# Performance work log

Hardware: AMD Instinct MI355X
Metric: run time of the kernel (lower is better)

The kernel has to match this reference:

```python
import jax, jax.numpy as jnp
import numpy as np

B, T, IN_DIM, OUT_DIM, H = 4096, 256, 64, 32, 128

def _linear_params(key, out_f, in_f):
    k1, k2 = jax.random.split(key)
    bound = 1.0 / np.sqrt(in_f)
    W = jax.random.uniform(k1, (out_f, in_f), jnp.float32, -bound, bound)
    b = jax.random.uniform(k2, (out_f,), jnp.float32, -bound, bound)
    return W, b

def _lstm_params(key, input_sz, hidden_sz):
    ks = jax.random.split(key, 4)
    bound = 1.0 / np.sqrt(hidden_sz)
    Wih = jax.random.uniform(ks[0], (4 * hidden_sz, input_sz), jnp.float32, -bound, bound)
    Whh = jax.random.uniform(ks[1], (4 * hidden_sz, hidden_sz), jnp.float32, -bound, bound)
    bih = jax.random.uniform(ks[2], (4 * hidden_sz,), jnp.float32, -bound, bound)
    bhh = jax.random.uniform(ks[3], (4 * hidden_sz,), jnp.float32, -bound, bound)
    return Wih, Whh, bih, bhh

def setup_inputs() -> dict:
    key = jax.random.key(0)
    ks = jax.random.split(key, 9)
    seq = jax.random.normal(ks[0], (B, T, IN_DIM), jnp.float32)
    h1 = jnp.zeros((B, H), jnp.float32); c1 = jnp.zeros((B, H), jnp.float32)
    h2 = jnp.zeros((B, H), jnp.float32); c2 = jnp.zeros((B, H), jnp.float32)
    W_in1, b_in1 = _linear_params(ks[1], 256, IN_DIM)
    W_in2, b_in2 = _linear_params(ks[2], 128, 256)
    W_in3, b_in3 = _linear_params(ks[3], 128, 128)
    Wih1, Whh1, bih1, bhh1 = _lstm_params(ks[4], 128, H)
    Wih2, Whh2, bih2, bhh2 = _lstm_params(ks[5], 128, H)
    W_out1, b_out1 = _linear_params(ks[6], 128, 128)
    W_out2, b_out2 = _linear_params(ks[7], 256, 128)
    W_out3, b_out3 = _linear_params(ks[8], OUT_DIM, 256)
    return dict(seq=seq, h1=h1, c1=c1, h2=h2, c2=c2,
                W_in1=W_in1, b_in1=b_in1, W_in2=W_in2, b_in2=b_in2, W_in3=W_in3, b_in3=b_in3,
                Wih1=Wih1, Whh1=Whh1, bih1=bih1, bhh1=bhh1,
                Wih2=Wih2, Whh2=Whh2, bih2=bih2, bhh2=bhh2,
                W_out1=W_out1, b_out1=b_out1, W_out2=W_out2, b_out2=b_out2, W_out3=W_out3, b_out3=b_out3)

def _lstm_cell(x, h, c, Wih, Whh, bih, bhh):
    # PyTorch LSTMCell: gates ordered i, f, g, o
    g = x @ Wih.T + bih + h @ Whh.T + bhh
    i, f, gg, o = jnp.split(g, 4, axis=-1)
    c_new = jax.nn.sigmoid(f) * c + jax.nn.sigmoid(i) * jnp.tanh(gg)
    h_new = jax.nn.sigmoid(o) * jnp.tanh(c_new)
    return h_new, c_new

def reference(seq, h1, c1, h2, c2,
              W_in1, b_in1, W_in2, b_in2, W_in3, b_in3,
              Wih1, Whh1, bih1, bhh1, Wih2, Whh2, bih2, bhh2,
              W_out1, b_out1, W_out2, b_out2, W_out3, b_out3):
    # fc_in applied to all timesteps at once (same math as per-step)
    x = jax.nn.relu(seq @ W_in1.T + b_in1)
    x = jax.nn.relu(x @ W_in2.T + b_in2)
    x = jax.nn.relu(x @ W_in3.T + b_in3)  # [B, T, 128]

    def step(carry, xt):
        h1, c1, h2, c2 = carry
        h1, c1 = _lstm_cell(xt, h1, c1, Wih1, Whh1, bih1, bhh1)
        h2, c2 = _lstm_cell(h1, h2, c2, Wih2, Whh2, bih2, bhh2)
        return (h1, c1, h2, c2), None

    (h1, c1, h2, c2), _ = jax.lax.scan(step, (h1, c1, h2, c2), jnp.swapaxes(x, 0, 1))

    y = jax.nn.relu(h2 @ W_out1.T + b_out1)
    y = jax.nn.relu(y @ W_out2.T + b_out2)
    return y @ W_out3.T + b_out3  # [B, out_dim]
```

## Files before the change

kernel.cpp:

```cpp
#include <hip/hip_runtime.h>


typedef unsigned short u16;
typedef short bf16x8 __attribute__((ext_vector_type(8)));
typedef float f32x4 __attribute__((ext_vector_type(4)));
typedef unsigned short u16x4 __attribute__((ext_vector_type(4)));

#define MFMA16(a, b, c) __builtin_amdgcn_mfma_f32_16x16x32_bf16((a), (b), (c), 0, 0, 0)

#define GLOAD_LDS(gp, lp) __builtin_amdgcn_global_load_lds( \
    (const __attribute__((address_space(1))) unsigned int*)(const void*)(gp), \
    (__attribute__((address_space(3))) unsigned int*)(void*)(lp), 16, 0, 0)

#define LGKM_BAR do { \
  asm volatile("s_waitcnt lgkmcnt(0)" ::: "memory"); \
  __builtin_amdgcn_sched_barrier(0); \
  __builtin_amdgcn_s_barrier(); \
  __builtin_amdgcn_sched_barrier(0); \
} while (0)

__device__ __forceinline__ u16 f2bf(float f) {
  union { float f; unsigned u; } v; v.f = f;
  return (u16)((v.u + 0x7FFFu + ((v.u >> 16) & 1u)) >> 16);
}
__device__ __forceinline__ float b2f(u16 v) {
  union { unsigned u; float f; } x; x.u = ((unsigned)v) << 16; return x.f;
}
__device__ __forceinline__ float fsig(float x) { return 1.0f / (1.0f + __expf(-x)); }
__device__ __forceinline__ float ftanh(float x) { return 2.0f / (1.0f + __expf(-2.0f * x)) - 1.0f; }

#define WHH1_U  0
#define WIH2_U  65536
#define WHH2_U  131072
#define WIH1_U  196608
#define W1_U    262144
#define W2_U    278528
#define W3_U    311296
#define WO1_U   327680
#define WO2_U   344064
#define WO3_U   376832
#define BS1_F   192512
#define BS2_F   193024
#define STH1_U  393216
#define STH2_U  917504
#define C1_F    720896
#define C2_F    1245184
#define G1X_U   4194304
#define TC      32
#define NCH     8


__global__ void prep_kernel(const float* __restrict__ Wih1, const float* __restrict__ Whh1,
                            const float* __restrict__ bih1, const float* __restrict__ bhh1,
                            const float* __restrict__ Wih2, const float* __restrict__ Whh2,
                            const float* __restrict__ bih2, const float* __restrict__ bhh2,
                            const float* __restrict__ W_in1, const float* __restrict__ W_in2,
                            const float* __restrict__ W_in3,
                            const float* __restrict__ W_out1, const float* __restrict__ W_out2,
                            const float* __restrict__ W_out3,
                            const float* __restrict__ h1_in, const float* __restrict__ h2_in,
                            const float* __restrict__ c1_in, const float* __restrict__ c2_in,
                            u16* __restrict__ wsu) {
  float* wsf = (float*)wsu;
  const int N_total = 2490368;
  int stride = gridDim.x * blockDim.x;
  for (int idx = blockIdx.x * blockDim.x + threadIdx.x; idx < N_total; idx += stride) {
    if (idx < 385024) {
      int within = idx & 511;
      int f = idx >> 9;
      int lane = within >> 3, e = within & 7;
      int lr = lane & 15, lg = lane >> 4;
      int k8 = lg * 8 + e;
      float v;
      if (f < 128) {
        int kf = f & 3, g = (f >> 2) & 3, w = f >> 4;
        v = Whh1[(g * 128 + w * 16 + lr) * 128 + kf * 32 + k8];
      } else if (f < 256) {
        int ff = f - 128; int kf = ff & 3, g = (ff >> 2) & 3, w = ff >> 4;
        v = Wih2[(g * 128 + w * 16 + lr) * 128 + kf * 32 + k8];
      } else if (f < 384) {
        int ff = f - 256; int kf = ff & 3, g = (ff >> 2) & 3, w = ff >> 4;
        v = Whh2[(g * 128 + w * 16 + lr) * 128 + kf * 32 + k8];
      } else if (f < 512) {
        int ff = f - 384; int kf = ff & 3, n = ff >> 2;
        v = Wih1[(n * 16 + lr) * 128 + kf * 32 + k8];
      } else if (f < 544) {
        int ff = f - 512; int kf = ff & 1, n = ff >> 1;
        v = W_in1[(n * 16 + lr) * 64 + kf * 32 + k8];
      } else if (f < 608) {
        int ff = f - 544; int kf = ff & 7, n = ff >> 3;
        v = W_in2[(n * 16 + lr) * 256 + kf * 32 + k8];
      } else if (f < 640) {
        int ff = f - 608; int kf = ff & 3, n = ff >> 2;
        v = W_in3[(n * 16 + lr) * 128 + kf * 32 + k8];
      } else if (f < 672) {
        int ff = f - 640; int kf = ff & 3, n = ff >> 2;
        v = W_out1[(n * 16 + lr) * 128 + kf * 32 + k8];
      } else if (f < 736) {
        int ff = f - 672; int kf = ff & 3, n = ff >> 2;
        v = W_out2[(n * 16 + lr) * 128 + kf * 32 + k8];
      } else {
        int ff = f - 736; int kf = ff & 7, n = ff >> 3;
        v = W_out3[(n * 16 + lr) * 256 + kf * 32 + k8];
      }
      wsu[idx] = f2bf(v);
    } else if (idx < 385536) {
      int i = idx - 385024; wsf[BS1_F + i] = bih1[i] + bhh1[i];
    } else if (idx < 386048) {
      int i = idx - 385536; wsf[BS2_F + i] = bih2[i] + bhh2[i];
    } else if (idx < 393216) {
    } else if (idx < 917504) {
      int i = idx - 393216; wsu[STH1_U + i] = f2bf(h1_in[i]);
    } else if (idx < 1441792) {
      int i = idx - 917504; wsu[STH2_U + i] = f2bf(h2_in[i]);
    } else if (idx < 1966080) {
      int i = idx - 1441792; wsf[C1_F + i] = c1_in[i];
    } else {
      int i = idx - 1966080; wsf[C2_F + i] = c2_in[i];
    }
  }
}

__global__ __launch_bounds__(256, 2)
void fc_chunk(const float* __restrict__ seq,
              const float* __restrict__ b_in1, const float* __restrict__ b_in2,
              const float* __restrict__ b_in3,
              u16* __restrict__ wsu, int t0) {
  __shared__ u16 SEQs[4096];
  __shared__ u16 F1s[16384];
  __shared__ u16 F2s[8192];
  __shared__ u16 XLs[8192];
  const int tid = threadIdx.x;
  const int wid = tid >> 6, lane = tid & 63;
  const int lr = lane & 15, lg = lane >> 4;
  const int bid_t = blockIdx.x & 1, bid_b = blockIdx.x >> 1;
  const int b0c = bid_b * 4, t0c = t0 + bid_t * 16;
  const float* bs1f = (const float*)wsu + BS1_F;

#pragma unroll
  for (int i = 0; i < 4; ++i) {
    int f = i * 1024 + tid * 4;
    int rho = f >> 6, k = f & 63;
    int b = b0c + (rho >> 4), tt = t0c + (rho & 15);
    float4 v = *(const float4*)(seq + ((size_t)b * 256 + tt) * 64 + k);
    u16x4 o = { f2bf(v.x), f2bf(v.y), f2bf(v.z), f2bf(v.w) };
    *(u16x4*)&SEQs[(rho * 64 + k) ^ ((rho & 7) << 3)] = o;
  }
  __syncthreads();

  {
    f32x4 a1[4][4] = {};
#pragma unroll
    for (int kf = 0; kf < 2; ++kf) {
      bf16x8 A[4];
#pragma unroll
      for (int rt = 0; rt < 4; ++rt) {
        int r = 16 * rt + lr;
        A[rt] = *(const bf16x8*)&SEQs[(r * 64 + (kf * 4 + lg) * 8) ^ ((r & 7) << 3)];
      }
#pragma unroll
      for (int n = 0; n < 4; ++n) {
        bf16x8 B = *(const bf16x8*)(wsu + W1_U + (size_t)(((4 * wid + n) * 2 + kf) * 512) + lane * 8);
#pragma unroll
        for (int rt = 0; rt < 4; ++rt) a1[rt][n] = MFMA16(A[rt], B, a1[rt][n]);
      }
    }
#pragma unroll
    for (int n = 0; n < 4; ++n) {
      float bb = b_in1[(4 * wid + n) * 16 + lr];
#pragma unroll
      for (int rt = 0; rt < 4; ++rt)
#pragma unroll
        for (int j = 0; j < 4; ++j) {
          int r = 16 * rt + lg * 4 + j, c = (4 * wid + n) * 16 + lr;
          F1s[(r * 256 + c) ^ ((r & 7) << 3)] = f2bf(fmaxf(a1[rt][n][j] + bb, 0.f));
        }
    }
  }
  __syncthreads();

  {
    f32x4 a2[4][2] = {};
#pragma unroll
    for (int kf = 0; kf < 8; ++kf) {
      bf16x8 A[4];
#pragma unroll
      for (int rt = 0; rt < 4; ++rt) {
        int r = 16 * rt + lr;
        A[rt] = *(const bf16x8*)&F1s[(r * 256 + (kf * 4 + lg) * 8) ^ ((r & 7) << 3)];
      }
#pragma unroll
      for (int n = 0; n < 2; ++n) {
        bf16x8 B = *(const bf16x8*)(wsu + W2_U + (size_t)(((2 * wid + n) * 8 + kf) * 512) + lane * 8);
#pragma unroll
        for (int rt = 0; rt < 4; ++rt) a2[rt][n] = MFMA16(A[rt], B, a2[rt][n]);
      }
    }
#pragma unroll
    for (int n = 0; n < 2; ++n) {
      float bb = b_in2[(2 * wid + n) * 16 + lr];
#pragma unroll
      for (int rt = 0; rt < 4; ++rt)
#pragma unroll
        for (int j = 0; j < 4; ++j) {
          int r = 16 * rt + lg * 4 + j, c = (2 * wid + n) * 16 + lr;
          F2s[(r * 128 + c) ^ ((r & 7) << 3)] = f2bf(fmaxf(a2[rt][n][j] + bb, 0.f));
        }
    }
  }
  __syncthreads();

  {
    f32x4 a3[4][2] = {};
#pragma unroll
    for (int kf = 0; kf < 4; ++kf) {
      bf16x8 A[4];
#pragma unroll
      for (int rt = 0; rt < 4; ++rt) {
        int r = 16 * rt + lr;
        A[rt] = *(const bf16x8*)&F2s[(r * 128 + (kf * 4 + lg) * 8) ^ ((r & 7) << 3)];
      }
#pragma unroll
      for (int n = 0; n < 2; ++n) {
        bf16x8 B = *(const bf16x8*)(wsu + W3_U + (size_t)(((2 * wid + n) * 4 + kf) * 512) + lane * 8);
#pragma unroll
        for (int rt = 0; rt < 4; ++rt) a3[rt][n] = MFMA16(A[rt], B, a3[rt][n]);
      }
    }
#pragma unroll
    for (int n = 0; n < 2; ++n) {
      float bb = b_in3[(2 * wid + n) * 16 + lr];
#pragma unroll
      for (int rt = 0; rt < 4; ++rt)
#pragma unroll
        for (int j = 0; j < 4; ++j) {
          int r = 16 * rt + lg * 4 + j, c = (2 * wid + n) * 16 + lr;
          XLs[(r * 128 + c) ^ ((r & 7) << 3)] = f2bf(fmaxf(a3[rt][n][j] + bb, 0.f));
        }
    }
  }
  __syncthreads();

  {
    f32x4 a4[4][8] = {};
#pragma unroll
    for (int kf = 0; kf < 4; ++kf) {
      bf16x8 A[4];
#pragma unroll
      for (int rt = 0; rt < 4; ++rt) {
        int r = 16 * rt + lr;
        A[rt] = *(const bf16x8*)&XLs[(r * 128 + (kf * 4 + lg) * 8) ^ ((r & 7) << 3)];
      }
#pragma unroll
      for (int n = 0; n < 8; ++n) {
        bf16x8 B = *(const bf16x8*)(wsu + WIH1_U + (size_t)(((wid * 8 + n) * 4 + kf) * 512) + lane * 8);
#pragma unroll
        for (int rt = 0; rt < 4; ++rt) a4[rt][n] = MFMA16(A[rt], B, a4[rt][n]);
      }
    }
    const int blk = bid_b >> 2, slg = bid_b & 3;
#pragma unroll
    for (int n = 0; n < 8; ++n) {
      float bb = bs1f[(wid * 8 + n) * 16 + lr];
#pragma unroll
      for (int j = 0; j < 4; ++j) {
        int tl = bid_t * 16 + lg * 4 + j;
        u16x4 o = { f2bf(a4[0][n][j] + bb), f2bf(a4[1][n][j] + bb),
                    f2bf(a4[2][n][j] + bb), f2bf(a4[3][n][j] + bb) };
        size_t au = (size_t)G1X_U +
            ((((((size_t)tl * 256 + blk) * 4 + slg) * 4 + wid) * 8 + n) * 16 + lr) * 4;
        *(u16x4*)(wsu + au) = o;
      }
    }
  }
}

__global__ __launch_bounds__(512, 1)
void scan_chunk(u16* __restrict__ wsu, float* __restrict__ out,
                const float* __restrict__ b_out1, const float* __restrict__ b_out2,
                const float* __restrict__ b_out3, int last) {
  __shared__ u16 Wl[65536];
  __shared__ u16 H1d[2][2048], H2d[2][2048];

  float* wsf = (float*)wsu;
  const int tid = threadIdx.x;
  const int wid = tid >> 6, lane = tid & 63;
  const int lr = lane & 15, lg = lane >> 4;
  const int b0 = blockIdx.x * 16;
  const int blkid = blockIdx.x;
  const int r5 = tid >> 5, c5 = (tid & 31) * 4;
  const int swl = (r5 * 128 + c5) ^ ((r5 & 7) << 3);

  bf16x8 wA[4][4], wB[4][4];
#pragma unroll
  for (int g = 0; g < 4; ++g)
#pragma unroll
    for (int kf = 0; kf < 4; ++kf) {
      wA[g][kf] = *(const bf16x8*)(wsu + WHH1_U + (size_t)(((wid * 4 + g) * 4 + kf) * 512) + lane * 8);
      wB[g][kf] = *(const bf16x8*)(wsu + WIH2_U + (size_t)(((wid * 4 + g) * 4 + kf) * 512) + lane * 8);
    }
#pragma unroll
  for (int g = 0; g < 4; ++g)
#pragma unroll
    for (int kf = 0; kf < 4; ++kf) {
      asm volatile("" : "+a"(wA[g][kf]));
      asm volatile("" : "+a"(wB[g][kf]));
    }

#pragma unroll
  for (int i = 0; i < 16; ++i)
    GLOAD_LDS(wsu + WHH2_U + wid * 8192 + i * 512 + lane * 8, &Wl[wid * 8192 + i * 512]);

  *(u16x4*)&H1d[0][swl] = *(const u16x4*)(wsu + STH1_U + (size_t)(b0 + r5) * 128 + c5);
  *(u16x4*)&H2d[0][swl] = *(const u16x4*)(wsu + STH2_U + (size_t)(b0 + r5) * 128 + c5);
  float cs1[4], cs2[4], bc2[4];
#pragma unroll
  for (int j = 0; j < 4; ++j) {
    cs1[j] = wsf[C1_F + (size_t)(b0 + lg * 4 + j) * 128 + 16 * wid + lr];
    cs2[j] = wsf[C2_F + (size_t)(b0 + lg * 4 + j) * 128 + 16 * wid + lr];
  }
#pragma unroll
  for (int g = 0; g < 4; ++g) bc2[g] = wsf[BS2_F + g * 128 + 16 * wid + lr];

  u16x4 gx[4];
#pragma unroll
  for (int g = 0; g < 4; ++g)
    gx[g] = *(const u16x4*)(wsu + G1X_U +
        ((((((size_t)0 * 256 + blkid) * 4 + lg) * 4 + g) * 8 + wid) * 16 + lr) * 4);

  __syncthreads();

  auto frag = [&](const u16* buf, int kg) -> bf16x8 {
    return *(const bf16x8*)&buf[(lr * 128 + kg * 8) ^ ((lr & 7) << 3)];
  };

#pragma unroll 2
  for (int tl = 0; tl < TC; ++tl) {
    const int p = tl & 1, q = p ^ 1;

    f32x4 acc[4];
#pragma unroll
    for (int g = 0; g < 4; ++g)
      acc[g] = (f32x4){ b2f(gx[g][0]), b2f(gx[g][1]), b2f(gx[g][2]), b2f(gx[g][3]) };
    if (tl < TC - 1) {
#pragma unroll
      for (int g = 0; g < 4; ++g)
        gx[g] = *(const u16x4*)(wsu + G1X_U +
            ((((((size_t)(tl + 1) * 256 + blkid) * 4 + lg) * 4 + g) * 8 + wid) * 16 + lr) * 4);
    }
    bf16x8 h1f[4];
#pragma unroll
    for (int kf = 0; kf < 4; ++kf) h1f[kf] = frag(H1d[p], kf * 4 + lg);
#pragma unroll
    for (int kf = 0; kf < 4; ++kf)
#pragma unroll
      for (int g = 0; g < 4; ++g) acc[g] = MFMA16(h1f[kf], wA[g][kf], acc[g]);
    u16 hv[4];
#pragma unroll
    for (int j = 0; j < 4; ++j) {
      float cn = fsig(acc[1][j]) * cs1[j] + fsig(acc[0][j]) * ftanh(acc[2][j]);
      cs1[j] = cn;
      hv[j] = f2bf(fsig(acc[3][j]) * ftanh(cn));
    }
#pragma unroll
    for (int j = 0; j < 4; ++j) {
      int r = lg * 4 + j;
      H1d[q][(r * 128 + 16 * wid + lr) ^ ((r & 7) << 3)] = hv[j];
    }
    LGKM_BAR;

    f32x4 acd[4];
#pragma unroll
    for (int g = 0; g < 4; ++g) acd[g] = (f32x4){ bc2[g], bc2[g], bc2[g], bc2[g] };
#pragma unroll
    for (int kf = 0; kf < 4; ++kf) {
      bf16x8 h1n = frag(H1d[q], kf * 4 + lg);
#pragma unroll
      for (int g = 0; g < 4; ++g) acd[g] = MFMA16(h1n, wB[g][kf], acd[g]);
    }
#pragma unroll
    for (int kf = 0; kf < 4; ++kf) {
      bf16x8 h2f = frag(H2d[p], kf * 4 + lg);
#pragma unroll
      for (int g = 0; g < 4; ++g) {
        bf16x8 B = *(const bf16x8*)&Wl[((wid * 16 + g * 4 + kf) * 512) + lane * 8];
        acd[g] = MFMA16(h2f, B, acd[g]);
      }
    }
#pragma unroll
    for (int j = 0; j < 4; ++j) {
      float cn = fsig(acd[1][j]) * cs2[j] + fsig(acd[0][j]) * ftanh(acd[2][j]);
      cs2[j] = cn;
      hv[j] = f2bf(fsig(acd[3][j]) * ftanh(cn));
    }
#pragma unroll
    for (int j = 0; j < 4; ++j) {
      int r = lg * 4 + j;
      H2d[q][(r * 128 + 16 * wid + lr) ^ ((r & 7) << 3)] = hv[j];
    }
  }
  LGKM_BAR;

  if (!last) {
    *(u16x4*)(wsu + STH1_U + (size_t)(b0 + r5) * 128 + c5) = *(const u16x4*)&H1d[0][swl];
    *(u16x4*)(wsu + STH2_U + (size_t)(b0 + r5) * 128 + c5) = *(const u16x4*)&H2d[0][swl];
#pragma unroll
    for (int j = 0; j < 4; ++j) {
      wsf[C1_F + (size_t)(b0 + lg * 4 + j) * 128 + 16 * wid + lr] = cs1[j];
      wsf[C2_F + (size_t)(b0 + lg * 4 + j) * 128 + 16 * wid + lr] = cs2[j];
    }
  } else {
    {
      f32x4 y1 = {};
#pragma unroll
      for (int kf = 0; kf < 4; ++kf) {
        bf16x8 A = frag(H2d[0], kf * 4 + lg);
        bf16x8 B = *(const bf16x8*)(wsu + WO1_U + (size_t)((wid * 4 + kf) * 512) + lane * 8);
        y1 = MFMA16(A, B, y1);
      }
      float bo1 = b_out1[wid * 16 + lr];
      LGKM_BAR;
#pragma unroll
      for (int j = 0; j < 4; ++j) {
        int r = lg * 4 + j;
        H1d[1][(r * 128 + 16 * wid + lr) ^ ((r & 7) << 3)] = f2bf(fmaxf(y1[j] + bo1, 0.f));
      }
      LGKM_BAR;
    }
    {
      f32x4 y2[2] = {};
#pragma unroll
      for (int kf = 0; kf < 4; ++kf) {
        bf16x8 A = frag(H1d[1], kf * 4 + lg);
#pragma unroll
        for (int n = 0; n < 2; ++n) {
          bf16x8 B = *(const bf16x8*)(wsu + WO2_U + (size_t)(((2 * wid + n) * 4 + kf) * 512) + lane * 8);
          y2[n] = MFMA16(A, B, y2[n]);
        }
      }
      LGKM_BAR;
#pragma unroll
      for (int n = 0; n < 2; ++n)
#pragma unroll
        for (int j = 0; j < 4; ++j) {
          int c = (2 * wid + n) * 16 + lr;
          float v = fmaxf(y2[n][j] + b_out2[c], 0.f);
          u16* buf = (c < 128) ? &H2d[1][0] : &H1d[0][0];
          int cc = c & 127, r = lg * 4 + j;
          buf[(r * 128 + cc) ^ ((r & 7) << 3)] = f2bf(v);
        }
      LGKM_BAR;
    }
    if (wid < 2) {
      f32x4 y3 = {};
#pragma unroll
      for (int kf = 0; kf < 8; ++kf) {
        const u16* ab = (kf < 4) ? &H2d[1][0] : &H1d[0][0];
        bf16x8 A = frag(ab, (kf & 3) * 4 + lg);
        bf16x8 B = *(const bf16x8*)(wsu + WO3_U + (size_t)((wid * 8 + kf) * 512) + lane * 8);
        y3 = MFMA16(A, B, y3);
      }
      float bo3 = b_out3[wid * 16 + lr];
#pragma unroll
      for (int j = 0; j < 4; ++j)
        out[(size_t)(b0 + lg * 4 + j) * 32 + wid * 16 + lr] = y3[j] + bo3;
    }
  }
}

extern "C" void kernel_launch(void* const* d_in, const int* in_sizes, int n_in,
                              void* d_out, int out_size, void* d_ws, size_t ws_size,
                              hipStream_t stream) {
  (void)in_sizes; (void)n_in; (void)out_size; (void)ws_size;
  const float* seq    = (const float*)d_in[0];
  const float* h1     = (const float*)d_in[1];
  const float* c1     = (const float*)d_in[2];
  const float* h2     = (const float*)d_in[3];
  const float* c2     = (const float*)d_in[4];
  const float* W_in1  = (const float*)d_in[5];
  const float* b_in1  = (const float*)d_in[6];
  const float* W_in2  = (const float*)d_in[7];
  const float* b_in2  = (const float*)d_in[8];
  const float* W_in3  = (const float*)d_in[9];
  const float* b_in3  = (const float*)d_in[10];
  const float* Wih1   = (const float*)d_in[11];
  const float* Whh1   = (const float*)d_in[12];
  const float* bih1   = (const float*)d_in[13];
  const float* bhh1   = (const float*)d_in[14];
  const float* Wih2   = (const float*)d_in[15];
  const float* Whh2   = (const float*)d_in[16];
  const float* bih2   = (const float*)d_in[17];
  const float* bhh2   = (const float*)d_in[18];
  const float* W_out1 = (const float*)d_in[19];
  const float* b_out1 = (const float*)d_in[20];
  const float* W_out2 = (const float*)d_in[21];
  const float* b_out2 = (const float*)d_in[22];
  const float* W_out3 = (const float*)d_in[23];
  const float* b_out3 = (const float*)d_in[24];
  u16* wsu = (u16*)d_ws;
  float* out = (float*)d_out;

  hipLaunchKernelGGL(prep_kernel, dim3(512), dim3(256), 0, stream,
                     Wih1, Whh1, bih1, bhh1, Wih2, Whh2, bih2, bhh2,
                     W_in1, W_in2, W_in3, W_out1, W_out2, W_out3,
                     h1, h2, c1, c2, wsu);
  for (int k = 0; k < NCH; ++k) {
    hipLaunchKernelGGL(fc_chunk, dim3(2048), dim3(256), 0, stream,
                       seq, b_in1, b_in2, b_in3, wsu, k * TC);
    hipLaunchKernelGGL(scan_chunk, dim3(256), dim3(512), 0, stream,
                       wsu, out, b_out1, b_out2, b_out3, (k == NCH - 1) ? 1 : 0);
  }
}
```

Before: 1.924 ms.

## Move LSTM1 input projection into scan kernel and reduce chunk count

The x@Wih1 projection moves out of the FC kernel and into the recurrent scan kernel. Wih1 fragments stay resident in registers and the bf16 FC output (128 wide) is streamed into LDS with prefetch two steps ahead. The per-step gate preload from a precomputed buffer is replaced by extra MFMAs. The launch uses one or two chunks depending on workspace size instead of eight, which removes launch and state save/restore overhead, but adds 16 MFMAs per step to the serial recurrence and more register pressure.

```diff
diff --git a/kernel.cpp b/kernel.cpp
--- a/kernel.cpp
+++ b/kernel.cpp
@@ -23,16 +23,13 @@
   union { float f; unsigned u; } v; v.f = f;
   return (u16)((v.u + 0x7FFFu + ((v.u >> 16) & 1u)) >> 16);
 }
-__device__ __forceinline__ float b2f(u16 v) {
-  union { unsigned u; float f; } x; x.u = ((unsigned)v) << 16; return x.f;
-}
 __device__ __forceinline__ float fsig(float x) { return 1.0f / (1.0f + __expf(-x)); }
 __device__ __forceinline__ float ftanh(float x) { return 2.0f / (1.0f + __expf(-2.0f * x)) - 1.0f; }
 
 #define WHH1_U  0
 #define WIH2_U  65536
-#define WHH2_U  131072
-#define WIH1_U  196608
+#define WIH1_U  131072
+#define WHH2_U  196608
 #define W1_U    262144
 #define W2_U    278528
 #define W3_U    311296
@@ -45,10 +42,7 @@
 #define STH2_U  917504
 #define C1_F    720896
 #define C2_F    1245184
-#define G1X_U   4194304
-#define TC      32
-#define NCH     8
-
+#define XBUF_U  4194304
 
 __global__ void prep_kernel(const float* __restrict__ Wih1, const float* __restrict__ Whh1,
                             const float* __restrict__ bih1, const float* __restrict__ bhh1,
@@ -72,18 +66,12 @@
       int lr = lane & 15, lg = lane >> 4;
       int k8 = lg * 8 + e;
       float v;
-      if (f < 128) {
-        int kf = f & 3, g = (f >> 2) & 3, w = f >> 4;
-        v = Whh1[(g * 128 + w * 16 + lr) * 128 + kf * 32 + k8];
-      } else if (f < 256) {
-        int ff = f - 128; int kf = ff & 3, g = (ff >> 2) & 3, w = ff >> 4;
-        v = Wih2[(g * 128 + w * 16 + lr) * 128 + kf * 32 + k8];
-      } else if (f < 384) {
-        int ff = f - 256; int kf = ff & 3, g = (ff >> 2) & 3, w = ff >> 4;
-        v = Whh2[(g * 128 + w * 16 + lr) * 128 + kf * 32 + k8];
-      } else if (f < 512) {
-        int ff = f - 384; int kf = ff & 3, n = ff >> 2;
-        v = Wih1[(n * 16 + lr) * 128 + kf * 32 + k8];
+      if (f < 512) {
+        int kf = f & 3, g = (f >> 2) & 3, w = (f >> 4) & 7;
+        int row = g * 128 + w * 16 + lr;
+        int k = kf * 32 + k8;
+        const float* M = (f < 128) ? Whh1 : (f < 256) ? Wih2 : (f < 384) ? Wih1 : Whh2;
+        v = M[row * 128 + k];
       } else if (f < 544) {
         int ff = f - 512; int kf = ff & 1, n = ff >> 1;
         v = W_in1[(n * 16 + lr) * 64 + kf * 32 + k8];
@@ -122,10 +110,10 @@
 }
 
 __global__ __launch_bounds__(256, 2)
-void fc_chunk(const float* __restrict__ seq,
-              const float* __restrict__ b_in1, const float* __restrict__ b_in2,
-              const float* __restrict__ b_in3,
-              u16* __restrict__ wsu, int t0) {
+void fc_all(const float* __restrict__ seq,
+            const float* __restrict__ b_in1, const float* __restrict__ b_in2,
+            const float* __restrict__ b_in3,
+            u16* __restrict__ wsu, int t0, int ntg) {
   __shared__ u16 SEQs[4096];
   __shared__ u16 F1s[16384];
   __shared__ u16 F2s[8192];
@@ -133,9 +121,8 @@
   const int tid = threadIdx.x;
   const int wid = tid >> 6, lane = tid & 63;
   const int lr = lane & 15, lg = lane >> 4;
-  const int bid_t = blockIdx.x & 1, bid_b = blockIdx.x >> 1;
+  const int bid_t = blockIdx.x % ntg, bid_b = blockIdx.x / ntg;
   const int b0c = bid_b * 4, t0c = t0 + bid_t * 16;
-  const float* bs1f = (const float*)wsu + BS1_F;
 
 #pragma unroll
   for (int i = 0; i < 4; ++i) {
@@ -242,44 +229,24 @@
   __syncthreads();
 
   {
-    f32x4 a4[4][8] = {};
-#pragma unroll
-    for (int kf = 0; kf < 4; ++kf) {
-      bf16x8 A[4];
-#pragma unroll
-      for (int rt = 0; rt < 4; ++rt) {
-        int r = 16 * rt + lr;
-        A[rt] = *(const bf16x8*)&XLs[(r * 128 + (kf * 4 + lg) * 8) ^ ((r & 7) << 3)];
-      }
-#pragma unroll
-      for (int n = 0; n < 8; ++n) {
-        bf16x8 B = *(const bf16x8*)(wsu + WIH1_U + (size_t)(((wid * 8 + n) * 4 + kf) * 512) + lane * 8);
-#pragma unroll
-        for (int rt = 0; rt < 4; ++rt) a4[rt][n] = MFMA16(A[rt], B, a4[rt][n]);
-      }
-    }
-    const int blk = bid_b >> 2, slg = bid_b & 3;
-#pragma unroll
-    for (int n = 0; n < 8; ++n) {
-      float bb = bs1f[(wid * 8 + n) * 16 + lr];
-#pragma unroll
-      for (int j = 0; j < 4; ++j) {
-        int tl = bid_t * 16 + lg * 4 + j;
-        u16x4 o = { f2bf(a4[0][n][j] + bb), f2bf(a4[1][n][j] + bb),
-                    f2bf(a4[2][n][j] + bb), f2bf(a4[3][n][j] + bb) };
-        size_t au = (size_t)G1X_U +
-            ((((((size_t)tl * 256 + blk) * 4 + slg) * 4 + wid) * 8 + n) * 16 + lr) * 4;
-        *(u16x4*)(wsu + au) = o;
-      }
+    int row = tid >> 2, seg = tid & 3;
+    int b = b0c + (row >> 4), tl = bid_t * 16 + (row & 15);
+    u16* dst = wsu + XBUF_U + ((size_t)tl * 4096 + b) * 128 + seg * 32;
+#pragma unroll
+    for (int g8 = 0; g8 < 4; ++g8) {
+      int c = seg * 32 + g8 * 8;
+      bf16x8 v = *(const bf16x8*)&XLs[(row * 128 + c) ^ ((row & 7) << 3)];
+      *(bf16x8*)(dst + g8 * 8) = v;
     }
   }
 }
 
 __global__ __launch_bounds__(512, 1)
-void scan_chunk(u16* __restrict__ wsu, float* __restrict__ out,
-                const float* __restrict__ b_out1, const float* __restrict__ b_out2,
-                const float* __restrict__ b_out3, int last) {
+void scan_kernel(u16* __restrict__ wsu, float* __restrict__ out,
+                 const float* __restrict__ b_out1, const float* __restrict__ b_out2,
+                 const float* __restrict__ b_out3, int nsteps, int last) {
   __shared__ u16 Wl[65536];
+  __shared__ u16 XB[2][2048];
   __shared__ u16 H1d[2][2048], H2d[2][2048];
 
   float* wsf = (float*)wsu;
@@ -287,17 +254,18 @@
   const int wid = tid >> 6, lane = tid & 63;
   const int lr = lane & 15, lg = lane >> 4;
   const int b0 = blockIdx.x * 16;
-  const int blkid = blockIdx.x;
   const int r5 = tid >> 5, c5 = (tid & 31) * 4;
   const int swl = (r5 * 128 + c5) ^ ((r5 & 7) << 3);
 
-  bf16x8 wA[4][4], wB[4][4];
+  bf16x8 wA[4][4], wB[4][4], wX[4][4];
 #pragma unroll
   for (int g = 0; g < 4; ++g)
 #pragma unroll
     for (int kf = 0; kf < 4; ++kf) {
-      wA[g][kf] = *(const bf16x8*)(wsu + WHH1_U + (size_t)(((wid * 4 + g) * 4 + kf) * 512) + lane * 8);
-      wB[g][kf] = *(const bf16x8*)(wsu + WIH2_U + (size_t)(((wid * 4 + g) * 4 + kf) * 512) + lane * 8);
+      size_t fo = (size_t)(((wid * 4 + g) * 4 + kf) * 512) + lane * 8;
+      wA[g][kf] = *(const bf16x8*)(wsu + WHH1_U + fo);
+      wB[g][kf] = *(const bf16x8*)(wsu + WIH2_U + fo);
+      wX[g][kf] = *(const bf16x8*)(wsu + WIH1_U + fo);
     }
 #pragma unroll
   for (int g = 0; g < 4; ++g)
@@ -305,29 +273,28 @@
     for (int kf = 0; kf < 4; ++kf) {
       asm volatile("" : "+a"(wA[g][kf]));
       asm volatile("" : "+a"(wB[g][kf]));
+      asm volatile("" : "+a"(wX[g][kf]));
     }
 
 #pragma unroll
   for (int i = 0; i < 16; ++i)
-    GLOAD_LDS(wsu + WHH2_U + wid * 8192 + i * 512 + lane * 8, &Wl[wid * 8192 + i * 512]);
+    GLOAD_LDS(wsu + WHH2_U + (wid * 16 + i) * 512 + lane * 8, &Wl[(wid * 16 + i) * 512]);
 
   *(u16x4*)&H1d[0][swl] = *(const u16x4*)(wsu + STH1_U + (size_t)(b0 + r5) * 128 + c5);
   *(u16x4*)&H2d[0][swl] = *(const u16x4*)(wsu + STH2_U + (size_t)(b0 + r5) * 128 + c5);
-  float cs1[4], cs2[4], bc2[4];
+  *(u16x4*)&XB[0][swl]  = *(const u16x4*)(wsu + XBUF_U + ((size_t)0 * 4096 + b0 + r5) * 128 + c5);
+  *(u16x4*)&XB[1][swl]  = *(const u16x4*)(wsu + XBUF_U + ((size_t)1 * 4096 + b0 + r5) * 128 + c5);
+  float cs1[4], cs2[4], bc1[4], bc2[4];
 #pragma unroll
   for (int j = 0; j < 4; ++j) {
     cs1[j] = wsf[C1_F + (size_t)(b0 + lg * 4 + j) * 128 + 16 * wid + lr];
     cs2[j] = wsf[C2_F + (size_t)(b0 + lg * 4 + j) * 128 + 16 * wid + lr];
   }
 #pragma unroll
-  for (int g = 0; g < 4; ++g) bc2[g] = wsf[BS2_F + g * 128 + 16 * wid + lr];
-
-  u16x4 gx[4];
-#pragma unroll
-  for (int g = 0; g < 4; ++g)
-    gx[g] = *(const u16x4*)(wsu + G1X_U +
-        ((((((size_t)0 * 256 + blkid) * 4 + lg) * 4 + g) * 8 + wid) * 16 + lr) * 4);
-
+  for (int g = 0; g < 4; ++g) {
+    bc1[g] = wsf[BS1_F + g * 128 + 16 * wid + lr];
+    bc2[g] = wsf[BS2_F + g * 128 + 16 * wid + lr];
+  }
   __syncthreads();
 
   auto frag = [&](const u16* buf, int kg) -> bf16x8 {
@@ -335,22 +302,24 @@
   };
 
 #pragma unroll 2
-  for (int tl = 0; tl < TC; ++tl) {
+  for (int tl = 0; tl < nsteps; ++tl) {
     const int p = tl & 1, q = p ^ 1;
+    int tn = tl + 2; if (tn > nsteps - 1) tn = nsteps - 1;
+    u16x4 xn = *(const u16x4*)(wsu + XBUF_U + ((size_t)tn * 4096 + b0 + r5) * 128 + c5);
 
     f32x4 acc[4];
 #pragma unroll
-    for (int g = 0; g < 4; ++g)
-      acc[g] = (f32x4){ b2f(gx[g][0]), b2f(gx[g][1]), b2f(gx[g][2]), b2f(gx[g][3]) };
-    if (tl < TC - 1) {
-#pragma unroll
-      for (int g = 0; g < 4; ++g)
-        gx[g] = *(const u16x4*)(wsu + G1X_U +
-            ((((((size_t)(tl + 1) * 256 + blkid) * 4 + lg) * 4 + g) * 8 + wid) * 16 + lr) * 4);
-    }
-    bf16x8 h1f[4];
-#pragma unroll
-    for (int kf = 0; kf < 4; ++kf) h1f[kf] = frag(H1d[p], kf * 4 + lg);
+    for (int g = 0; g < 4; ++g) acc[g] = (f32x4){ bc1[g], bc1[g], bc1[g], bc1[g] };
+    bf16x8 xf[4], h1f[4];
+#pragma unroll
+    for (int kf = 0; kf < 4; ++kf) {
+      xf[kf]  = frag(XB[p], kf * 4 + lg);
+      h1f[kf] = frag(H1d[p], kf * 4 + lg);
+    }
+#pragma unroll
+    for (int kf = 0; kf < 4; ++kf)
+#pragma unroll
+      for (int g = 0; g < 4; ++g) acc[g] = MFMA16(xf[kf], wX[g][kf], acc[g]);
 #pragma unroll
     for (int kf = 0; kf < 4; ++kf)
 #pragma unroll
@@ -383,7 +352,7 @@
       bf16x8 h2f = frag(H2d[p], kf * 4 + lg);
 #pragma unroll
       for (int g = 0; g < 4; ++g) {
-        bf16x8 B = *(const bf16x8*)&Wl[((wid * 16 + g * 4 + kf) * 512) + lane * 8];
+        bf16x8 B = *(const bf16x8*)&Wl[(((wid * 4 + g) * 4 + kf) * 512) + lane * 8];
         acd[g] = MFMA16(h2f, B, acd[g]);
       }
     }
@@ -398,6 +367,7 @@
       int r = lg * 4 + j;
       H2d[q][(r * 128 + 16 * wid + lr) ^ ((r & 7) << 3)] = hv[j];
     }
+    *(u16x4*)&XB[p][swl] = xn;
   }
   LGKM_BAR;
 
@@ -471,7 +441,7 @@
 extern "C" void kernel_launch(void* const* d_in, const int* in_sizes, int n_in,
                               void* d_out, int out_size, void* d_ws, size_t ws_size,
                               hipStream_t stream) {
-  (void)in_sizes; (void)n_in; (void)out_size; (void)ws_size;
+  (void)in_sizes; (void)n_in; (void)out_size;
   const float* seq    = (const float*)d_in[0];
   const float* h1     = (const float*)d_in[1];
   const float* c1     = (const float*)d_in[2];
@@ -500,14 +470,19 @@
   u16* wsu = (u16*)d_ws;
   float* out = (float*)d_out;
 
+  const size_t need1 = 8388608ull + (size_t)256 * 4096 * 128 * 2;
+  const int nch = (ws_size >= need1) ? 1 : 2;
+  const int tc = 256 / nch;
+  const int ntg = tc / 16;
+
   hipLaunchKernelGGL(prep_kernel, dim3(512), dim3(256), 0, stream,
                      Wih1, Whh1, bih1, bhh1, Wih2, Whh2, bih2, bhh2,
                      W_in1, W_in2, W_in3, W_out1, W_out2, W_out3,
                      h1, h2, c1, c2, wsu);
-  for (int k = 0; k < NCH; ++k) {
-    hipLaunchKernelGGL(fc_chunk, dim3(2048), dim3(256), 0, stream,
-                       seq, b_in1, b_in2, b_in3, wsu, k * TC);
-    hipLaunchKernelGGL(scan_chunk, dim3(256), dim3(512), 0, stream,
-                       wsu, out, b_out1, b_out2, b_out3, (k == NCH - 1) ? 1 : 0);
+  for (int k = 0; k < nch; ++k) {
+    hipLaunchKernelGGL(fc_all, dim3(1024 * ntg), dim3(256), 0, stream,
+                       seq, b_in1, b_in2, b_in3, wsu, k * tc, ntg);
+    hipLaunchKernelGGL(scan_kernel, dim3(256), dim3(512), 0, stream,
+                       wsu, out, b_out1, b_out2, b_out3, tc, (k == nch - 1) ? 1 : 0);
   }
 }
```

After: 1.908 ms. Within noise of the previous version (-0.9%).
